# Optimization experiments

Hardware: AMD Instinct MI355X
Metric: run time of the kernel (lower is better)

## Reference

```python
import jax, jax.numpy as jnp
import numpy as np

ROPE_THETA = 10000.0
NH, D_NOPE, D_ROPE, D_V = 16, 128, 64, 128
D_QK = D_NOPE + D_ROPE  # 192
KV_LORA = 512
SCALING = D_QK ** -0.5
EPS = 1e-6


def rmsnorm(x, w):
    xf = x.astype(jnp.float32)
    var = jnp.mean(xf * xf, axis=-1, keepdims=True)
    return (w * (xf * jax.lax.rsqrt(var + EPS))).astype(x.dtype)


def rotate_half(x):
    x1, x2 = jnp.split(x, 2, axis=-1)
    return jnp.concatenate([-x2, x1], axis=-1)


def rope_cos_sin(seq_len, dim, dtype):
    inv_freq = 1.0 / (ROPE_THETA ** (jnp.arange(0, dim, 2, dtype=jnp.float32) / dim))
    t = jnp.arange(seq_len, dtype=jnp.float32)
    ang = jnp.outer(t, inv_freq)              # [S, dim/2]
    emb = jnp.concatenate([ang, ang], axis=-1)  # [S, dim]
    return jnp.cos(emb).astype(dtype), jnp.sin(emb).astype(dtype)


def setup_inputs() -> dict:
    key = jax.random.key(0)
    ks = jax.random.split(key, 8)
    B, S, H, QLR = 2, 2048, 2048, 1536
    s = lambda k, shape, fan: jax.random.normal(k, shape, jnp.float32) * (fan ** -0.5)
    return {
        "hidden_states": jax.random.normal(ks[0], (B, S, H), jnp.float32),
        "q_a_w": s(ks[1], (QLR, H), H),
        "q_a_ln_w": jnp.ones((QLR,), jnp.float32),
        "q_b_w": s(ks[2], (NH * D_QK, QLR), QLR),
        "kv_a_w": s(ks[3], (KV_LORA + D_ROPE, H), H),
        "kv_a_ln_w": jnp.ones((KV_LORA,), jnp.float32),
        "kv_b_w": s(ks[4], (NH * (D_NOPE + D_V), KV_LORA), KV_LORA),
        "o_w": s(ks[5], (H, NH * D_V), NH * D_V),
    }


def reference(hidden_states, q_a_w, q_a_ln_w, q_b_w, kv_a_w, kv_a_ln_w, kv_b_w, o_w):
    B, S, H = hidden_states.shape
    # --- Q path: low-rank compression -> norm -> up-proj ---
    q_a = hidden_states @ q_a_w.T                         # [B,S,QLR]
    q = rmsnorm(q_a, q_a_ln_w) @ q_b_w.T                  # [B,S,NH*D_QK]
    q = q.reshape(B, S, NH, D_QK).transpose(0, 2, 1, 3)   # [B,NH,S,D_QK]
    q_nope, q_rope = q[..., :D_NOPE], q[..., D_NOPE:]
    # --- KV path: joint compression with MQA rope branch ---
    kv_a = hidden_states @ kv_a_w.T                       # [B,S,KV_LORA+D_ROPE]
    c_kv, k_rope = kv_a[..., :KV_LORA], kv_a[..., KV_LORA:]
    kv = rmsnorm(c_kv, kv_a_ln_w) @ kv_b_w.T              # [B,S,NH*(D_NOPE+D_V)]
    kv = kv.reshape(B, S, NH, D_NOPE + D_V).transpose(0, 2, 1, 3)
    k_nope, v = kv[..., :D_NOPE], kv[..., D_NOPE:]        # [B,NH,S,*]
    k_rope = k_rope[:, None, :, :]                        # [B,1,S,D_ROPE] shared across heads
    # --- decoupled RoPE on rope sub-dims only ---
    cos, sin = rope_cos_sin(S, D_ROPE, hidden_states.dtype)
    q_rope = q_rope * cos + rotate_half(q_rope) * sin
    k_rope = k_rope * cos + rotate_half(k_rope) * sin
    k_rope = jnp.broadcast_to(k_rope, (B, NH, S, D_ROPE))
    q_full = jnp.concatenate([q_nope, q_rope], axis=-1)   # [B,NH,S,D_QK]
    k_full = jnp.concatenate([k_nope, k_rope], axis=-1)
    # --- causal attention ---
    scores = jnp.einsum("bhqd,bhkd->bhqk", q_full, k_full) * SCALING
    causal = jnp.tril(jnp.ones((S, S), bool))
    scores = jnp.where(causal, scores, jnp.finfo(scores.dtype).min)
    attn = jax.nn.softmax(scores.astype(jnp.float32), axis=-1).astype(v.dtype)
    out = jnp.einsum("bhqk,bhkd->bhqd", attn, v)          # [B,NH,S,D_V]
    out = out.transpose(0, 2, 1, 3).reshape(B, S, NH * D_V)
    return out @ o_w.T                                    # [B,S,H]
```

## Files before the change

### kernel.cpp

```cpp
#include <hip/hip_runtime.h>
#include <hip/hip_bf16.h>
#include <math.h>
#include <stdint.h>

#define NHEADS 16
#define DQK 192
#define DVDIM 128
#define SEQ 2048
#define BATCH 2
#define MROWS 4096
#define HDIM 2048
#define QLORA 1536
#define KVLORA 512
#define SCALING 0.07216878364870323f
#define NTQ 32

typedef __attribute__((ext_vector_type(8))) short short8;
typedef __attribute__((ext_vector_type(4))) short short4v;
typedef __attribute__((ext_vector_type(4))) float f32x4;

__device__ __forceinline__ float4 ld4(const float* p) {
    return *reinterpret_cast<const float4*>(p);
}
__device__ __forceinline__ unsigned short f2b(float x) {
    __hip_bfloat16 h = __float2bfloat16(x);
    return __builtin_bit_cast(unsigned short, h);
}
__device__ __forceinline__ void gload16(const void* g, void* l) {
    typedef const __attribute__((address_space(1))) unsigned int ga_t;
    typedef __attribute__((address_space(3))) unsigned int ls_t;
    __builtin_amdgcn_global_load_lds((ga_t*)(uintptr_t)g, (ls_t*)(uintptr_t)l, 16, 0, 0);
}

__global__ __launch_bounds__(256) void cvt_bf(const float* __restrict__ in,
                                              unsigned short* __restrict__ o, int n8) {
    int i = blockIdx.x * 256 + threadIdx.x;
    if (i >= n8) return;
    float4 a = ld4(in + (size_t)i * 8), b = ld4(in + (size_t)i * 8 + 4);
    short8 t;
    t[0] = (short)f2b(a.x); t[1] = (short)f2b(a.y); t[2] = (short)f2b(a.z); t[3] = (short)f2b(a.w);
    t[4] = (short)f2b(b.x); t[5] = (short)f2b(b.y); t[6] = (short)f2b(b.z); t[7] = (short)f2b(b.w);
    *(short8*)(o + (size_t)i * 8) = t;
}

template <int MODE>
__global__ __launch_bounds__(256) void gemm_bf16(
        const unsigned short* __restrict__ A, int lda,
        const unsigned short* __restrict__ W, const unsigned short* __restrict__ W2,
        float* __restrict__ Cf, int ldc,
        unsigned short* __restrict__ O1, unsigned short* __restrict__ O2,
        const float* __restrict__ cosb, const float* __restrict__ sinb,
        int K) {
    __shared__ unsigned short As[3][128 * 32];
    __shared__ unsigned short Bs[3][128 * 32];

    const int tid = threadIdx.x;
    const int bm = blockIdx.y * 128, bn = blockIdx.x * 128;
    const int w = tid >> 6, lane = tid & 63;
    const int wr = (w >> 1) * 64, wc = (w & 1) * 64;
    const int fr = lane & 15, fq = lane >> 4;

    const int r0 = w * 32 + (lane >> 2);
    const int c0 = (lane & 3) * 8;

    const unsigned short* Ag0;
    if constexpr (MODE == 4) {
        Ag0 = A + (size_t)((bm >> 7) * 256 + 128 + r0) * lda + c0;
    } else {
        Ag0 = A + (size_t)(bm + r0) * lda + c0;
    }
    const unsigned short* Ag1 = Ag0 + (size_t)16 * lda;

    const unsigned short* Wg0;
    const unsigned short* Wg1;
    if constexpr (MODE == 1) {
        if (bn < 1536) {
            Wg0 = W + (size_t)(bn + r0) * K + c0;
            Wg1 = Wg0 + (size_t)16 * K;
        } else {
            int br0 = bn - 1536 + r0;      if (br0 > 575) br0 = 575;
            int br1 = bn - 1536 + r0 + 16; if (br1 > 575) br1 = 575;
            Wg0 = W2 + (size_t)br0 * K + c0;
            Wg1 = W2 + (size_t)br1 * K + c0;
        }
    } else if constexpr (MODE == 3) {
        Wg0 = W + (size_t)((bn >> 7) * 256 + r0) * K + c0;
        Wg1 = Wg0 + (size_t)16 * K;
    } else {
        Wg0 = W + (size_t)(bn + r0) * K + c0;
        Wg1 = Wg0 + (size_t)16 * K;
    }

#define STAGE(buf, koff) do { \
        gload16(Ag0 + (koff), &As[buf][(w * 32) * 32]); \
        gload16(Ag1 + (koff), &As[buf][(w * 32 + 16) * 32]); \
        gload16(Wg0 + (koff), &Bs[buf][(w * 32) * 32]); \
        gload16(Wg1 + (koff), &Bs[buf][(w * 32 + 16) * 32]); \
    } while (0)

    f32x4 acc[4][4];
    #pragma unroll
    for (int m = 0; m < 4; m++)
        #pragma unroll
        for (int n = 0; n < 4; n++) acc[m][n] = (f32x4)0.0f;

    const int NT = K >> 5;
    STAGE(0, 0);
    STAGE(1, 32);
    int cb = 0;
    for (int t = 0; t < NT; t++) {
        if (t == NT - 1) asm volatile("s_waitcnt vmcnt(0)" ::: "memory");
        else             asm volatile("s_waitcnt vmcnt(4)" ::: "memory");
        __builtin_amdgcn_s_barrier();
        __builtin_amdgcn_sched_barrier(0);

        if (t + 2 < NT) {
            int nb = cb + 2; if (nb >= 3) nb -= 3;
            STAGE(nb, (t + 2) * 32);
        }

        short8 af[4], bfr[4];
        #pragma unroll
        for (int m = 0; m < 4; m++)
            af[m] = *(const short8*)&As[cb][(wr + m * 16 + fr) * 32 + fq * 8];
        #pragma unroll
        for (int n = 0; n < 4; n++)
            bfr[n] = *(const short8*)&Bs[cb][(wc + n * 16 + fr) * 32 + fq * 8];
        #pragma unroll
        for (int m = 0; m < 4; m++)
            #pragma unroll
            for (int n = 0; n < 4; n++)
                acc[m][n] = __builtin_amdgcn_mfma_f32_16x16x32_bf16(af[m], bfr[n], acc[m][n], 0, 0, 0);

        cb++; if (cb >= 3) cb = 0;
    }
#undef STAGE

    if constexpr (MODE == 0) {
        #pragma unroll
        for (int m = 0; m < 4; m++)
            #pragma unroll
            for (int n = 0; n < 4; n++) {
                const int col = bn + wc + n * 16 + fr;
                #pragma unroll
                for (int j = 0; j < 4; j++)
                    Cf[(size_t)(bm + wr + m * 16 + fq * 4 + j) * ldc + col] = acc[m][n][j];
            }
    } else if constexpr (MODE == 1) {
        #pragma unroll
        for (int m = 0; m < 4; m++)
            #pragma unroll
            for (int n = 0; n < 4; n++) {
                const int col = bn + wc + n * 16 + fr;
                if (col < 2112) {
                    #pragma unroll
                    for (int j = 0; j < 4; j++)
                        Cf[(size_t)(bm + wr + m * 16 + fq * 4 + j) * 2112 + col] = acc[m][n][j];
                }
            }
    } else if constexpr (MODE == 2) {
        #pragma unroll
        for (int n = 0; n < 4; n++) {
            const int col = bn + wc + n * 16 + fr;
            const int h = col / DQK, d = col % DQK;
            #pragma unroll
            for (int m = 0; m < 4; m++) {
                #pragma unroll
                for (int j = 0; j < 4; j++) {
                    const int row = bm + wr + m * 16 + fq * 4 + j;
                    const int s = row & (SEQ - 1), b = row >> 11;
                    float v = acc[m][n][j];
                    if (d >= DVDIM) {
                        const int j5 = d - DVDIM;
                        const float partner = acc[m][n ^ 2][j];
                        const float rot = (j5 < 32) ? -partner : partner;
                        v = v * cosb[s * 64 + j5] + rot * sinb[s * 64 + j5];
                    }
                    O1[((size_t)(b * NHEADS + h) * SEQ + s) * DQK + d] = f2b(v);
                }
            }
        }
    } else if constexpr (MODE == 3) {
        #pragma unroll
        for (int n = 0; n < 4; n++) {
            const int col = bn + wc + n * 16 + fr;
            const int h = col >> 7, d = col & 127;
            #pragma unroll
            for (int m = 0; m < 4; m++) {
                #pragma unroll
                for (int j = 0; j < 4; j++) {
                    const int row = bm + wr + m * 16 + fq * 4 + j;
                    const int s = row & (SEQ - 1);
                    const int bh = (row >> 11) * NHEADS + h;
                    O1[((size_t)bh * SEQ + s) * DQK + d] = f2b(acc[m][n][j]);
                }
            }
        }
    } else {
        #pragma unroll
        for (int n = 0; n < 4; n++) {
            const int col = bn + wc + n * 16 + fr;
            const int b = col >> 11, s = col & (SEQ - 1);
            #pragma unroll
            for (int m = 0; m < 4; m++) {
                #pragma unroll
                for (int j = 0; j < 4; j++) {
                    const int vf = bm + wr + m * 16 + fq * 4 + j;
                    const int h = vf >> 7, dv = vf & 127;
                    O2[((size_t)(b * NHEADS + h) * DVDIM + dv) * SEQ + s] = f2b(acc[m][n][j]);
                }
            }
        }
    }
}

__global__ __launch_bounds__(256) void rmsnorm_bf(const float* __restrict__ x,
                                                  const float* __restrict__ w,
                                                  unsigned short* __restrict__ o,
                                                  int ncols, int instride) {
    const float* xr = x + (size_t)blockIdx.x * instride;
    unsigned short* orow = o + (size_t)blockIdx.x * ncols;
    const int tid = threadIdx.x;
    float ss = 0.f;
    for (int c = tid * 4; c < ncols; c += 1024) {
        float4 v = ld4(xr + c);
        ss += v.x * v.x + v.y * v.y + v.z * v.z + v.w * v.w;
    }
    #pragma unroll
    for (int d = 32; d > 0; d >>= 1) ss += __shfl_down(ss, d);
    __shared__ float wsum[4];
    if ((tid & 63) == 0) wsum[tid >> 6] = ss;
    __syncthreads();
    float total = wsum[0] + wsum[1] + wsum[2] + wsum[3];
    float scale = 1.0f / sqrtf(total / (float)ncols + 1e-6f);
    for (int c = tid * 4; c < ncols; c += 1024) {
        float4 v = ld4(xr + c);
        short4v t;
        t[0] = (short)f2b(v.x * scale * w[c + 0]);
        t[1] = (short)f2b(v.y * scale * w[c + 1]);
        t[2] = (short)f2b(v.z * scale * w[c + 2]);
        t[3] = (short)f2b(v.w * scale * w[c + 3]);
        *(short4v*)&orow[c] = t;
    }
}

__global__ void rope_table(float* __restrict__ cost, float* __restrict__ sint) {
    int s = blockIdx.x, j = threadIdx.x;
    int i = j & 31;
    float inv = 1.0f / powf(10000.0f, (float)i * (1.0f / 32.0f));
    float ang = (float)s * inv;
    cost[s * 64 + j] = cosf(ang);
    sint[s * 64 + j] = sinf(ang);
}

__global__ void rope_k_bcast(const float* __restrict__ qkva,
                             const float* __restrict__ cost,
                             const float* __restrict__ sint,
                             unsigned short* __restrict__ kbf) {
    const int r = blockIdx.x;
    const int j = threadIdx.x;
    const int b = r >> 11, s = r & (SEQ - 1);
    const float* base = qkva + (size_t)r * 2112 + 2048;
    const float x = base[j];
    const float rot = (j < 32) ? -base[j + 32] : base[j - 32];
    const unsigned short v = f2b(x * cost[s * 64 + j] + rot * sint[s * 64 + j]);
    #pragma unroll
    for (int h = 0; h < NHEADS; h++)
        kbf[((size_t)(b * NHEADS + h) * SEQ + s) * DQK + DVDIM + j] = v;
}

__global__ __launch_bounds__(256, 2) void flash_mfma(const unsigned short* __restrict__ qbf,
                                                     const unsigned short* __restrict__ kbf,
                                                     const unsigned short* __restrict__ vbfT,
                                                     unsigned short* __restrict__ attn) {
    __shared__ unsigned short Ks[64][200];
    __shared__ unsigned short Vs[128][72];
    __shared__ unsigned short Ps[4][16][72];

    const int lin = blockIdx.x;
    const int xcd = lin & 7;
    const int idx = lin >> 3;
    const int bh = xcd * 4 + (idx >> 4);
    const int bx = idx & 15;
    const int b = bh >> 4, h = bh & 15;
    const int tid = threadIdx.x;
    const int w = tid >> 6, lane = tid & 63;
    const int fr = lane & 15, fq = lane >> 4;

    const unsigned short* Qh = qbf + ((size_t)bh * SEQ) * DQK;
    const unsigned short* Kh = kbf + ((size_t)bh * SEQ) * DQK;
    const unsigned short* Vh = vbfT + ((size_t)bh * 128) * SEQ;

    short8 kreg[6], vreg[4];
    #pragma unroll
    for (int u = 0; u < 6; u++) {
        int i = tid + u * 256;
        int row = i / 24, c = (i % 24) * 8;
        kreg[u] = *(const short8*)(Kh + (size_t)row * DQK + c);
    }
    #pragma unroll
    for (int u = 0; u < 4; u++) {
        int i = tid + u * 256;
        int row = i >> 3, c = (i & 7) * 8;
        vreg[u] = *(const short8*)(Vh + (size_t)row * SEQ + c);
    }

    #pragma unroll 1
    for (int pass = 0; pass < 2; pass++) {
        const int qt = pass ? (NTQ - 1 - bx) : bx;
        const int q0 = qt * 64;

        short8 qf[6];
        {
            const unsigned short* qrow = Qh + (size_t)(q0 + w * 16 + fr) * DQK;
            #pragma unroll
            for (int kw = 0; kw < 6; kw++)
                qf[kw] = *(const short8*)(qrow + kw * 32 + fq * 8);
        }

        f32x4 acc[8];
        #pragma unroll
        for (int n = 0; n < 8; n++) acc[n] = (f32x4)0.0f;
        float mrow[4], lrow[4];
        #pragma unroll
        for (int j = 0; j < 4; j++) { mrow[j] = -3.0e38f; lrow[j] = 0.0f; }

        #pragma unroll 1
        for (int t = 0; t <= qt; t++) {
            __syncthreads();
            #pragma unroll
            for (int u = 0; u < 6; u++) {
                int i = tid + u * 256;
                int row = i / 24, c = (i % 24) * 8;
                *(short8*)&Ks[row][c] = kreg[u];
            }
            #pragma unroll
            for (int u = 0; u < 4; u++) {
                int i = tid + u * 256;
                int row = i >> 3, c = (i & 7) * 8;
                *(short8*)&Vs[row][c] = vreg[u];
            }
            __syncthreads();

            const int nt = (t < qt) ? (t + 1) : (pass == 0 ? 0 : -1);
            if (nt >= 0) {
                const int kt0n = nt * 64;
                #pragma unroll
                for (int u = 0; u < 6; u++) {
                    int i = tid + u * 256;
                    int row = i / 24, c = (i % 24) * 8;
                    kreg[u] = *(const short8*)(Kh + (size_t)(kt0n + row) * DQK + c);
                }
                #pragma unroll
                for (int u = 0; u < 4; u++) {
                    int i = tid + u * 256;
                    int row = i >> 3, c = (i & 7) * 8;
                    vreg[u] = *(const short8*)(Vh + (size_t)row * SEQ + kt0n + c);
                }
            }

            f32x4 sfr[4];
            #pragma unroll
            for (int n = 0; n < 4; n++) sfr[n] = (f32x4)0.0f;
            __builtin_amdgcn_s_setprio(1);
            #pragma unroll
            for (int kw = 0; kw < 6; kw++) {
                #pragma unroll
                for (int n = 0; n < 4; n++) {
                    short8 kf = *(const short8*)&Ks[n * 16 + fr][kw * 32 + fq * 8];
                    sfr[n] = __builtin_amdgcn_mfma_f32_16x16x32_bf16(qf[kw], kf, sfr[n], 0, 0, 0);
                }
            }
            __builtin_amdgcn_s_setprio(0);

            const bool diag = (t == qt);
            float pv[4][4];
            float tmax[4];
            #pragma unroll
            for (int j = 0; j < 4; j++) tmax[j] = -3.0e38f;
            #pragma unroll
            for (int n = 0; n < 4; n++) {
                #pragma unroll
                for (int j = 0; j < 4; j++) {
                    float s = sfr[n][j] * SCALING;
                    if (diag && (n * 16 + fr > w * 16 + fq * 4 + j)) s = -3.0e38f;
                    pv[n][j] = s;
                    tmax[j] = fmaxf(tmax[j], s);
                }
            }
            #pragma unroll
            for (int j = 0; j < 4; j++) {
                tmax[j] = fmaxf(tmax[j], __shfl_xor(tmax[j], 1));
                tmax[j] = fmaxf(tmax[j], __shfl_xor(tmax[j], 2));
                tmax[j] = fmaxf(tmax[j], __shfl_xor(tmax[j], 4));
                tmax[j] = fmaxf(tmax[j], __shfl_xor(tmax[j], 8));
            }
            bool defer[4];
            float mnew[4], es[4], psum[4];
            #pragma unroll
            for (int j = 0; j < 4; j++) {
                defer[j] = (tmax[j] - mrow[j] <= 8.0f);
                mnew[j] = defer[j] ? mrow[j] : tmax[j];
                es[j] = defer[j] ? 1.0f : __expf(mrow[j] - mnew[j]);
                psum[j] = 0.0f;
            }
            #pragma unroll
            for (int n = 0; n < 4; n++) {
                #pragma unroll
                for (int j = 0; j < 4; j++) {
                    float p = __expf(pv[n][j] - mnew[j]);
                    pv[n][j] = p;
                    psum[j] += p;
                }
            }
            #pragma unroll
            for (int j = 0; j < 4; j++) {
                psum[j] += __shfl_xor(psum[j], 1);
                psum[j] += __shfl_xor(psum[j], 2);
                psum[j] += __shfl_xor(psum[j], 4);
                psum[j] += __shfl_xor(psum[j], 8);
                lrow[j] = lrow[j] * es[j] + psum[j];
                mrow[j] = mnew[j];
            }
            const bool needresc = !(defer[0] && defer[1] && defer[2] && defer[3]);
            if (__any(needresc)) {
                #pragma unroll
                for (int n = 0; n < 8; n++) {
                    #pragma unroll
                    for (int j = 0; j < 4; j++) acc[n][j] *= es[j];
                }
            }
            #pragma unroll
            for (int n = 0; n < 4; n++) {
                #pragma unroll
                for (int j = 0; j < 4; j++)
                    Ps[w][fq * 4 + j][n * 16 + fr] = f2b(pv[n][j]);
            }
            __builtin_amdgcn_s_setprio(1);
            #pragma unroll
            for (int tt = 0; tt < 2; tt++) {
                short8 pa = *(const short8*)&Ps[w][fr][tt * 32 + fq * 8];
                #pragma unroll
                for (int n = 0; n < 8; n++) {
                    short8 vf = *(const short8*)&Vs[n * 16 + fr][tt * 32 + fq * 8];
                    acc[n] = __builtin_amdgcn_mfma_f32_16x16x32_bf16(pa, vf, acc[n], 0, 0, 0);
                }
            }
            __builtin_amdgcn_s_setprio(0);
        }

        #pragma unroll
        for (int j = 0; j < 4; j++) {
            const float inv = 1.0f / lrow[j];
            unsigned short* orow = attn + (size_t)(b * SEQ + q0 + w * 16 + fq * 4 + j) * (NHEADS * DVDIM) + h * DVDIM;
            #pragma unroll
            for (int n = 0; n < 8; n++)
                orow[n * 16 + fr] = f2b(acc[n][j] * inv);
        }
    }
}

extern "C" void kernel_launch(void* const* d_in, const int* in_sizes, int n_in,
                              void* d_out, int out_size, void* d_ws, size_t ws_size,
                              hipStream_t stream) {
    const float* hidden   = (const float*)d_in[0];
    const float* q_a_w    = (const float*)d_in[1];
    const float* q_a_ln_w = (const float*)d_in[2];
    const float* q_b_w    = (const float*)d_in[3];
    const float* kv_a_w   = (const float*)d_in[4];
    const float* kv_a_ln_w= (const float*)d_in[5];
    const float* kv_b_w   = (const float*)d_in[6];
    const float* o_w      = (const float*)d_in[7];
    float* out = (float*)d_out;

    char* base = (char*)d_ws;
    size_t off = 0;
    auto alloc = [&](size_t bytes) -> void* {
        void* p = base + off;
        off += (bytes + 255) & ~(size_t)255;
        return p;
    };
    float* qkva          = (float*)alloc((size_t)MROWS * 2112 * 4);
    float* cosb          = (float*)alloc((size_t)SEQ * 64 * 4);
    float* sinb          = (float*)alloc((size_t)SEQ * 64 * 4);
    unsigned short* hbf  = (unsigned short*)alloc((size_t)MROWS * HDIM * 2);
    unsigned short* w_qa = (unsigned short*)alloc((size_t)QLORA * HDIM * 2);
    unsigned short* w_qb = (unsigned short*)alloc((size_t)3072 * QLORA * 2);
    unsigned short* w_kva= (unsigned short*)alloc((size_t)576 * HDIM * 2);
    unsigned short* w_kvb= (unsigned short*)alloc((size_t)4096 * KVLORA * 2);
    unsigned short* w_o  = (unsigned short*)alloc((size_t)HDIM * 2048 * 2);
    unsigned short* qabf = (unsigned short*)alloc((size_t)MROWS * QLORA * 2);
    unsigned short* ckvbf= (unsigned short*)alloc((size_t)MROWS * KVLORA * 2);
    unsigned short* qbf  = (unsigned short*)alloc((size_t)32 * SEQ * DQK * 2);
    unsigned short* kbf  = (unsigned short*)alloc((size_t)32 * SEQ * DQK * 2);
    unsigned short* vbfT = (unsigned short*)alloc((size_t)32 * DVDIM * SEQ * 2);
    unsigned short* attnbf=(unsigned short*)alloc((size_t)MROWS * 2048 * 2);

    cvt_bf<<<4096, 256, 0, stream>>>(hidden, hbf, 1048576);
    cvt_bf<<<1536, 256, 0, stream>>>(q_a_w,  w_qa, 393216);
    cvt_bf<<<2304, 256, 0, stream>>>(q_b_w,  w_qb, 589824);
    cvt_bf<<< 576, 256, 0, stream>>>(kv_a_w, w_kva, 147456);
    cvt_bf<<<1024, 256, 0, stream>>>(kv_b_w, w_kvb, 262144);
    cvt_bf<<<2048, 256, 0, stream>>>(o_w,    w_o,  524288);
    rope_table<<<SEQ, 64, 0, stream>>>(cosb, sinb);

    gemm_bf16<1><<<dim3(17, 32), 256, 0, stream>>>(hbf, HDIM, w_qa, w_kva,
                                                   qkva, 2112, nullptr, nullptr,
                                                   nullptr, nullptr, HDIM);
    rmsnorm_bf<<<MROWS, 256, 0, stream>>>(qkva, q_a_ln_w, qabf, QLORA, 2112);
    rmsnorm_bf<<<MROWS, 256, 0, stream>>>(qkva + 1536, kv_a_ln_w, ckvbf, KVLORA, 2112);
    gemm_bf16<2><<<dim3(24, 32), 256, 0, stream>>>(qabf, QLORA, w_qb, nullptr,
                                                   nullptr, 0, qbf, nullptr,
                                                   cosb, sinb, QLORA);
    gemm_bf16<3><<<dim3(16, 32), 256, 0, stream>>>(ckvbf, KVLORA, w_kvb, nullptr,
                                                   nullptr, 0, kbf, nullptr,
                                                   nullptr, nullptr, KVLORA);
    gemm_bf16<4><<<dim3(32, 16), 256, 0, stream>>>(w_kvb, KVLORA, ckvbf, nullptr,
                                                   nullptr, 0, nullptr, vbfT,
                                                   nullptr, nullptr, KVLORA);
    rope_k_bcast<<<MROWS, 64, 0, stream>>>(qkva, cosb, sinb, kbf);
    flash_mfma<<<512, 256, 0, stream>>>(qbf, kbf, vbfT, attnbf);
    gemm_bf16<0><<<dim3(16, 32), 256, 0, stream>>>(attnbf, 2048, w_o, nullptr,
                                                   out, 2048, nullptr, nullptr,
                                                   nullptr, nullptr, 2048);
}
```

Baseline: 488.3 us.

## Swizzle GEMM LDS tiles and merge six bf16 conversions into one launch

```diff
diff --git a/kernel.cpp b/kernel.cpp
--- a/kernel.cpp
+++ b/kernel.cpp
@@ -32,15 +32,32 @@
     __builtin_amdgcn_global_load_lds((ga_t*)(uintptr_t)g, (ls_t*)(uintptr_t)l, 16, 0, 0);
 }
 
-__global__ __launch_bounds__(256) void cvt_bf(const float* __restrict__ in,
-                                              unsigned short* __restrict__ o, int n8) {
-    int i = blockIdx.x * 256 + threadIdx.x;
-    if (i >= n8) return;
-    float4 a = ld4(in + (size_t)i * 8), b = ld4(in + (size_t)i * 8 + 4);
+#define S0 1048576
+#define S1 393216
+#define S2 589824
+#define S3 147456
+#define S4 262144
+#define S5 524288
+__global__ __launch_bounds__(256) void cvt_all(
+        const float* __restrict__ i0, const float* __restrict__ i1,
+        const float* __restrict__ i2, const float* __restrict__ i3,
+        const float* __restrict__ i4, const float* __restrict__ i5,
+        unsigned short* __restrict__ o0, unsigned short* __restrict__ o1,
+        unsigned short* __restrict__ o2, unsigned short* __restrict__ o3,
+        unsigned short* __restrict__ o4, unsigned short* __restrict__ o5) {
+    size_t i = (size_t)blockIdx.x * 256 + threadIdx.x;
+    const float* in; unsigned short* out;
+    if      (i < S0)                  { in = i0; out = o0; }
+    else if (i < S0+S1)               { in = i1; out = o1; i -= S0; }
+    else if (i < S0+S1+S2)            { in = i2; out = o2; i -= S0+S1; }
+    else if (i < S0+S1+S2+S3)         { in = i3; out = o3; i -= S0+S1+S2; }
+    else if (i < S0+S1+S2+S3+S4)      { in = i4; out = o4; i -= S0+S1+S2+S3; }
+    else                              { in = i5; out = o5; i -= S0+S1+S2+S3+S4; }
+    float4 a = ld4(in + i * 8), b = ld4(in + i * 8 + 4);
     short8 t;
     t[0] = (short)f2b(a.x); t[1] = (short)f2b(a.y); t[2] = (short)f2b(a.z); t[3] = (short)f2b(a.w);
     t[4] = (short)f2b(b.x); t[5] = (short)f2b(b.y); t[6] = (short)f2b(b.z); t[7] = (short)f2b(b.w);
-    *(short8*)(o + (size_t)i * 8) = t;
+    *(short8*)(out + i * 8) = t;
 }
 
 template <int MODE>
@@ -60,8 +77,10 @@
     const int wr = (w >> 1) * 64, wc = (w & 1) * 64;
     const int fr = lane & 15, fq = lane >> 4;
 
-    const int r0 = w * 32 + (lane >> 2);
-    const int c0 = (lane & 3) * 8;
+    const int lr = lane >> 2;
+    const int swzw = (lr & 3) ^ ((lr >> 2) & 3);
+    const int r0 = w * 32 + lr;
+    const int c0 = (((lane & 3) ^ swzw)) * 8;
 
     const unsigned short* Ag0;
     if constexpr (MODE == 4) {
@@ -104,6 +123,9 @@
         #pragma unroll
         for (int n = 0; n < 4; n++) acc[m][n] = (f32x4)0.0f;
 
+    const int swzr = (fr & 3) ^ ((fr >> 2) & 3);
+    const int fqs = (fq ^ swzr) * 8;
+
     const int NT = K >> 5;
     STAGE(0, 0);
     STAGE(1, 32);
@@ -122,10 +144,10 @@
         short8 af[4], bfr[4];
         #pragma unroll
         for (int m = 0; m < 4; m++)
-            af[m] = *(const short8*)&As[cb][(wr + m * 16 + fr) * 32 + fq * 8];
+            af[m] = *(const short8*)&As[cb][(wr + m * 16 + fr) * 32 + fqs];
         #pragma unroll
         for (int n = 0; n < 4; n++)
-            bfr[n] = *(const short8*)&Bs[cb][(wc + n * 16 + fr) * 32 + fq * 8];
+            bfr[n] = *(const short8*)&Bs[cb][(wc + n * 16 + fr) * 32 + fqs];
         #pragma unroll
         for (int m = 0; m < 4; m++)
             #pragma unroll
@@ -496,12 +518,8 @@
     unsigned short* vbfT = (unsigned short*)alloc((size_t)32 * DVDIM * SEQ * 2);
     unsigned short* attnbf=(unsigned short*)alloc((size_t)MROWS * 2048 * 2);
 
-    cvt_bf<<<4096, 256, 0, stream>>>(hidden, hbf, 1048576);
-    cvt_bf<<<1536, 256, 0, stream>>>(q_a_w,  w_qa, 393216);
-    cvt_bf<<<2304, 256, 0, stream>>>(q_b_w,  w_qb, 589824);
-    cvt_bf<<< 576, 256, 0, stream>>>(kv_a_w, w_kva, 147456);
-    cvt_bf<<<1024, 256, 0, stream>>>(kv_b_w, w_kvb, 262144);
-    cvt_bf<<<2048, 256, 0, stream>>>(o_w,    w_o,  524288);
+    cvt_all<<<11584, 256, 0, stream>>>(hidden, q_a_w, q_b_w, kv_a_w, kv_b_w, o_w,
+                                       hbf, w_qa, w_qb, w_kva, w_kvb, w_o);
     rope_table<<<SEQ, 64, 0, stream>>>(cosb, sinb);
 
     gemm_bf16<1><<<dim3(17, 32), 256, 0, stream>>>(hbf, HDIM, w_qa, w_kva,
```

Result: faster. 465.9 us (-4.6%).
